# Kernel tuning notes

Hardware: AMD Instinct MI355X
Metric: run time of the kernel (lower is better)

The kernel has to match this reference:

```python
import jax, jax.numpy as jnp
import numpy as np

B, N, D_IN, D_OUT, H, W = 2, 2048, 1024, 1024, 16, 64
DH = D_OUT // H


def setup_inputs() -> dict:
    key = jax.random.key(0)
    ks = jax.random.split(key, 6)
    x = jax.random.normal(ks[0], (B, N, D_IN), dtype=jnp.float32)
    s_in = 1.0 / np.sqrt(D_IN)
    s_out = 1.0 / np.sqrt(D_OUT)
    wq = jax.random.normal(ks[1], (D_IN, D_OUT), dtype=jnp.float32) * s_in
    wk = jax.random.normal(ks[2], (D_IN, D_OUT), dtype=jnp.float32) * s_in
    wv = jax.random.normal(ks[3], (D_IN, D_OUT), dtype=jnp.float32) * s_in
    wo = jax.random.normal(ks[4], (D_OUT, D_OUT), dtype=jnp.float32) * s_out
    # sparse global tokens: every 256th token is global
    global_attention = (jnp.arange(N)[None, :] % 256 == 0) & jnp.ones((B, 1), bool)
    return {"x": x, "wq": wq, "wk": wk, "wv": wv, "wo": wo,
            "global_attention": global_attention}


def _mask(global_attention):
    # True = masked out. Causal local window + global rows/cols unmasked.
    i = jnp.arange(N)[:, None]
    j = jnp.arange(N)[None, :]
    allowed = (i - j < W) & (i >= j)          # causal sliding window
    local_mask = ~allowed                      # [N, N], True = masked
    g = global_attention                       # [B, N] bool
    # global token j clears row j and column j of the mask
    global_clear = g[:, :, None] | g[:, None, :]   # [B, N, N]
    return local_mask[None, :, :] & ~global_clear  # [B, N, N]


def reference(x, wq, wk, wv, wo, global_attention):
    b, n, _ = x.shape
    q = (x @ wq).reshape(b, n, H, DH).transpose(0, 2, 1, 3)  # [b,h,n,dh]
    k = (x @ wk).reshape(b, n, H, DH).transpose(0, 2, 1, 3)
    v = (x @ wv).reshape(b, n, H, DH).transpose(0, 2, 1, 3)
    scores = jnp.einsum('bhqd,bhkd->bhqk', q, k) / jnp.sqrt(jnp.float32(DH))
    mask = _mask(global_attention)[:, None, :, :]            # [b,1,n,n]
    scores = jnp.where(mask, -jnp.inf, scores)
    attn = jax.nn.softmax(scores, axis=-1)
    ctx = jnp.einsum('bhqk,bhkd->bqhd', attn, v).reshape(b, n, D_OUT)
    return ctx @ wo
```

## Files before the change

### kernel.cpp

```cpp
#include <hip/hip_runtime.h>


using u16 = unsigned short;
using u32 = unsigned int;

typedef __attribute__((ext_vector_type(8))) short bf16x8;
typedef __attribute__((ext_vector_type(4))) float f32x4;

__device__ __forceinline__ float b2f(u16 s) {
  union { u32 u; float f; } x; x.u = ((u32)s) << 16; return x.f;
}
__device__ __forceinline__ u16 f2b(float f) {
  union { float f; u32 u; } x; x.f = f;
  u32 r = (x.u + 0x7fffu + ((x.u >> 16) & 1u)) >> 16;
  return (u16)r;
}

__global__ __launch_bounds__(256) void k_pre(const float* __restrict__ x,
                                             u16* __restrict__ xb,
                                             const float* __restrict__ wq,
                                             const float* __restrict__ wk,
                                             const float* __restrict__ wv,
                                             const float* __restrict__ wo,
                                             u16* __restrict__ wqkvT,
                                             u16* __restrict__ woT) {
  __shared__ float tile[64][65];
  const int bid = blockIdx.x;
  if (bid < 2048) {
    int idx = (bid * 256 + threadIdx.x) * 8;
    float4 a = *(const float4*)(x + idx);
    float4 b = *(const float4*)(x + idx + 4);
    uint4 o;
    o.x = (u32)f2b(a.x) | ((u32)f2b(a.y) << 16);
    o.y = (u32)f2b(a.z) | ((u32)f2b(a.w) << 16);
    o.z = (u32)f2b(b.x) | ((u32)f2b(b.y) << 16);
    o.w = (u32)f2b(b.z) | ((u32)f2b(b.w) << 16);
    *(uint4*)(xb + idx) = o;
  } else {
    const int id = bid - 2048;
    const int z = id >> 8, xy = id & 255;
    const float* src = (z == 0) ? wq : (z == 1) ? wk : (z == 2) ? wv : wo;
    u16* dst = (z < 3) ? (wqkvT + ((size_t)z << 20)) : woT;
    const int n0 = (xy & 15) * 64, k0 = (xy >> 4) * 64;
    const int tx = threadIdx.x & 63, ty = threadIdx.x >> 6;
    #pragma unroll
    for (int r = 0; r < 64; r += 4)
      tile[r + ty][tx] = src[(size_t)(k0 + r + ty) * 1024 + n0 + tx];
    __syncthreads();
    #pragma unroll
    for (int r = 0; r < 64; r += 4)
      dst[(size_t)(n0 + r + ty) * 1024 + k0 + tx] = f2b(tile[tx][r + ty]);
  }
}

__device__ __forceinline__ void gload16(const u16* g, u16* l) {
  __builtin_amdgcn_global_load_lds((const __attribute__((address_space(1))) void*)g,
                                   (__attribute__((address_space(3))) void*)l, 16, 0, 0);
}

__global__ __launch_bounds__(512, 2) void k_qkv256(const u16* __restrict__ A,
                                                   const u16* __restrict__ Bt,
                                                   u16* __restrict__ C) {
  __shared__ __attribute__((aligned(16))) u16 lds[65536];
  const int K = 1024, N = 3072, NT = 16;
  const int t = threadIdx.x;
  const int wid = t >> 6, lane = t & 63;
  const int l4 = lane >> 4, l16 = lane & 15;
  const int qr = wid >> 2, qc = wid & 3;
  const int d = blockIdx.y * gridDim.x + blockIdx.x;
  const int qq = (gridDim.x * gridDim.y) >> 3;
  const int tau = (d & 7) * qq + (d >> 3);
  const int bn = tau % gridDim.x, bm = tau / gridDim.x;
  const u16* Ab = A + (size_t)bm * 256 * K;
  const u16* Bb = Bt + (size_t)bn * 256 * K;
  const int rowbase = wid * 8 + (lane >> 3);
  const int scc = ((lane & 7) ^ ((lane >> 3) & 7)) << 3;
  const int sdst = wid << 6;
  const int rsw = (l16 & 7);
  f32x4 acc[2][2][4][2] = {};
  bf16x8 af[4][2], bf0[2][2], bf1[2][2];

  #define STG(G, BUF, KT, H)                                                       \
    { const u16* gb = (G) ? Bb : Ab;                                               \
      u16* lb = lds + ((G) ? 32768 : 0) + (BUF) * 16384 + ((H) * 1024 + sdst) * 8; \
      _Pragma("unroll")                                                            \
      for (int i = 0; i < 2; ++i)                                                  \
        gload16(gb + (size_t)((H) * 128 + i * 64 + rowbase) * K + (KT) * 64 + scc, \
                lb + i * 4096); }

  #define LOAD_A(AS, MH)                                                           \
    { _Pragma("unroll")                                                            \
      for (int m = 0; m < 4; ++m) {                                                \
        const int ro = (MH) * 128 + qr * 64 + m * 16 + l16;                        \
        _Pragma("unroll")                                                          \
        for (int ks = 0; ks < 2; ++ks)                                             \
          af[m][ks] = *(const bf16x8*)&(AS)[ro * 64 + (((ks * 4 + l4) ^ rsw) << 3)]; \
      } }

  #define LOAD_B(BS, BF, NH)                                                       \
    { _Pragma("unroll")                                                            \
      for (int n = 0; n < 2; ++n) {                                                \
        const int ro = (NH) * 128 + qc * 32 + n * 16 + l16;                        \
        _Pragma("unroll")                                                          \
        for (int ks = 0; ks < 2; ++ks)                                             \
          BF[n][ks] = *(const bf16x8*)&(BS)[ro * 64 + (((ks * 4 + l4) ^ rsw) << 3)]; \
      } }

  #define QUAD(MH, NH, BF)                                                         \
    { __builtin_amdgcn_s_setprio(1);                                               \
      _Pragma("unroll")                                                            \
      for (int m = 0; m < 4; ++m)                                                  \
        _Pragma("unroll")                                                          \
        for (int n = 0; n < 2; ++n) {                                              \
          f32x4 c = acc[MH][NH][m][n];                                             \
          c = __builtin_amdgcn_mfma_f32_16x16x32_bf16(af[m][0], BF[n][0], c, 0, 0, 0); \
          c = __builtin_amdgcn_mfma_f32_16x16x32_bf16(af[m][1], BF[n][1], c, 0, 0, 0); \
          acc[MH][NH][m][n] = c;                                                   \
        }                                                                          \
      __builtin_amdgcn_s_setprio(0); }

  STG(0, 0, 0, 0); STG(1, 0, 0, 0); STG(0, 0, 0, 1); STG(1, 0, 0, 1);
  STG(0, 1, 1, 0); STG(1, 1, 1, 0);
  asm volatile("s_waitcnt vmcnt(4)" ::: "memory");
  __builtin_amdgcn_s_barrier();

  for (int tt = 0; tt < NT; ++tt) {
    const int beta = tt & 1;
    const u16* As = lds + beta * 16384;
    const u16* Bs = lds + 32768 + beta * 16384;
    LOAD_A(As, 0);
    LOAD_B(Bs, bf0, 0);
    if (tt + 1 < NT) STG(0, beta ^ 1, tt + 1, 1);
    __builtin_amdgcn_s_barrier();
    QUAD(0, 0, bf0);
    __builtin_amdgcn_s_barrier();
    LOAD_B(Bs, bf1, 1);
    if (tt + 1 < NT) STG(1, beta ^ 1, tt + 1, 1);
    __builtin_amdgcn_s_barrier();
    QUAD(0, 1, bf1);
    __builtin_amdgcn_s_barrier();
    LOAD_A(As, 1);
    if (tt + 2 < NT) STG(0, beta, tt + 2, 0);
    __builtin_amdgcn_s_barrier();
    QUAD(1, 0, bf0);
    __builtin_amdgcn_s_barrier();
    if (tt + 2 < NT) STG(1, beta, tt + 2, 0);
    __builtin_amdgcn_s_barrier();
    QUAD(1, 1, bf1);
    if (tt + 2 < NT)      asm volatile("s_waitcnt vmcnt(4)" ::: "memory");
    else if (tt + 1 < NT) asm volatile("s_waitcnt vmcnt(0)" ::: "memory");
    __builtin_amdgcn_s_barrier();
  }
  #undef STG
  #undef LOAD_A
  #undef LOAD_B
  #undef QUAD

  #pragma unroll
  for (int mh = 0; mh < 2; ++mh)
    #pragma unroll
    for (int m = 0; m < 4; ++m) {
      const int row0 = bm * 256 + mh * 128 + qr * 64 + m * 16 + l4 * 4;
      #pragma unroll
      for (int nh = 0; nh < 2; ++nh)
        #pragma unroll
        for (int n = 0; n < 2; ++n) {
          const int col = bn * 256 + nh * 128 + qc * 32 + n * 16 + l16;
          #pragma unroll
          for (int r = 0; r < 4; ++r)
            C[(size_t)(row0 + r) * N + col] = f2b(acc[mh][nh][m][n][r]);
        }
    }
}

template<int F32OUT, int GRED>
__global__ __launch_bounds__(256, 2) void k_gemm64(const u16* __restrict__ A,
                                                   const u16* __restrict__ Bt,
                                                   void* __restrict__ C, int N, int K,
                                                   const float* __restrict__ gpart,
                                                   u16* __restrict__ ctxw) {
  __shared__ u16 lds[3][6144];
  const int t = threadIdx.x;
  const int wid = t >> 6, lane = t & 63;
  const int l4 = lane >> 4, l16 = lane & 15;
  const int wr = wid >> 1, wc = wid & 1;
  const int d = blockIdx.y * gridDim.x + blockIdx.x;
  const int qq = (gridDim.x * gridDim.y) >> 3;
  const int tau = (d & 7) * qq + (d >> 3);
  const int bn = tau % gridDim.x, bm = tau / gridDim.x;
  const u16* Ab = A + (size_t)bm * 64 * K;
  const u16* Bb = Bt + (size_t)bn * 128 * K;
  const int srow0 = t >> 2;
  const int scol = (((t & 3) ^ ((t >> 3) & 3)) << 3);
  const int sdst = wid << 9;
  const int sl8 = ((l4 ^ ((l16 >> 1) & 3)) << 3);
  const int NT = K >> 5;
  f32x4 acc[2][4] = {};

  if (GRED && (bm & 3) == 0) {
    const int bb = bm >> 5;
    const int irow = (bm & 31) * 64;
    const int row8 = (bm & 31) >> 2;
    const int h = t >> 4;
    const int d0 = (t & 15) * 4;
    const float* g0 = gpart + ((size_t)(bb * 16 + h) * 32) * 520;
    float o0 = 0.f, o1 = 0.f, o2 = 0.f, o3 = 0.f, ls = 0.f;
    for (int q = 0; q < 32; ++q) {
      const float4 v = *(const float4*)(g0 + q * 520 + row8 * 64 + d0);
      o0 += v.x; o1 += v.y; o2 += v.z; o3 += v.w;
      ls += g0[q * 520 + 512 + row8];
    }
    const float inv = 1.f / ls;
    u16* cw = ctxw + ((size_t)(bb * 2048 + irow)) * 1024 + h * 64 + d0;
    cw[0] = f2b(o0 * inv); cw[1] = f2b(o1 * inv);
    cw[2] = f2b(o2 * inv); cw[3] = f2b(o3 * inv);
    __syncthreads();
  }

  #pragma unroll
  for (int pt = 0; pt < 2; ++pt) {
    gload16(Ab + (size_t)srow0 * K + (pt << 5) + scol, &lds[pt][sdst]);
    #pragma unroll
    for (int c = 0; c < 2; ++c)
      gload16(Bb + (size_t)(c * 64 + srow0) * K + (pt << 5) + scol,
              &lds[pt][2048 + c * 2048 + sdst]);
  }

  int cur = 0, nxt2 = 2;
  for (int tt = 0; tt < NT; ++tt) {
    if (tt + 1 < NT) asm volatile("s_waitcnt vmcnt(3)" ::: "memory");
    else             asm volatile("s_waitcnt vmcnt(0)" ::: "memory");
    __builtin_amdgcn_s_barrier();
    if (tt + 2 < NT) {
      const int k0 = (tt + 2) << 5;
      u16* dst = &lds[nxt2][0];
      gload16(Ab + (size_t)srow0 * K + k0 + scol, dst + sdst);
      #pragma unroll
      for (int c = 0; c < 2; ++c)
        gload16(Bb + (size_t)(c * 64 + srow0) * K + k0 + scol, dst + 2048 + c * 2048 + sdst);
    }
    const u16* As = lds[cur];
    const u16* Bs = lds[cur] + 2048;
    bf16x8 af[2], bf[4];
    #pragma unroll
    for (int m = 0; m < 2; ++m)
      af[m] = *(const bf16x8*)&As[(wr * 32 + m * 16 + l16) * 32 + sl8];
    #pragma unroll
    for (int n = 0; n < 4; ++n)
      bf[n] = *(const bf16x8*)&Bs[(wc * 64 + n * 16 + l16) * 32 + sl8];
    __builtin_amdgcn_s_setprio(1);
    #pragma unroll
    for (int m = 0; m < 2; ++m)
      #pragma unroll
      for (int n = 0; n < 4; ++n)
        acc[m][n] = __builtin_amdgcn_mfma_f32_16x16x32_bf16(af[m], bf[n], acc[m][n], 0, 0, 0);
    __builtin_amdgcn_s_setprio(0);
    cur = (cur == 2) ? 0 : cur + 1;
    nxt2 = (nxt2 == 2) ? 0 : nxt2 + 1;
  }

  #pragma unroll
  for (int m = 0; m < 2; ++m) {
    const int row0 = bm * 64 + wr * 32 + m * 16 + l4 * 4;
    #pragma unroll
    for (int n = 0; n < 4; ++n) {
      const int col = bn * 128 + wc * 64 + n * 16 + l16;
      #pragma unroll
      for (int r = 0; r < 4; ++r) {
        if (F32OUT) ((float*)C)[(size_t)(row0 + r) * N + col] = acc[m][n][r];
        else        ((u16*)C)[(size_t)(row0 + r) * N + col] = f2b(acc[m][n][r]);
      }
    }
  }
}

__global__ __launch_bounds__(256) void k_attn_tile(const u16* __restrict__ qkv,
                                                   u16* __restrict__ ctx,
                                                   float* __restrict__ gpart) {
  __shared__ u16 buf[26880];
  __shared__ u16 Qgs[16 * 72];
  __shared__ u16 Pgs[16 * 72];
  __shared__ float lred[4][16];
  u16* Qs = buf;
  u16* Ks = buf + 4608;
  u16* Vt = buf + 16128;
  u16* Ps = buf;

  const int t = threadIdx.x, wid = t >> 6, lane = t & 63;
  const int l4 = lane >> 4, l16 = lane & 15;
  const int qt = blockIdx.x, h = blockIdx.y, b = blockIdx.z;
  const int q0 = qt * 64;
  const int kbase = q0 - 64;
  const size_t base = (size_t)b * 2048 * 3072;
  const u16* Qg = qkv + base + h * 64;
  const u16* Kg = qkv + base + 1024 + h * 64;
  const u16* Vg = qkv + base + 2048 + h * 64;

  for (int s = t; s < 512; s += 256) {
    int r = s >> 3, c = (s & 7) * 8;
    *(uint4*)&Qs[r * 72 + c] = *(const uint4*)&Qg[(size_t)(q0 + r) * 3072 + c];
  }
  if (t < 128) {
    int r = t >> 3, c = (t & 7) * 8;
    if (r < 8) {
      *(uint4*)&Qgs[r * 72 + c] = *(const uint4*)&Qg[(size_t)(r * 256) * 3072 + c];
    } else {
      uint4 z = {0, 0, 0, 0};
      *(uint4*)&Qgs[r * 72 + c] = z;
    }
  }
  for (int s = t; s < 1088; s += 256) {
    int r = s >> 3, c = (s & 7) * 8;
    int j = (r < 128) ? max(kbase + r, 0) : (r - 128) * 256;
    *(uint4*)&Ks[r * 72 + c] = *(const uint4*)&Kg[(size_t)j * 3072 + c];
  }
  for (int s = t; s < 1088; s += 256) {
    int r = s >> 3, c = (s & 7) * 8;
    int j = (r < 128) ? max(kbase + r, 0) : (r - 128) * 256;
    uint4 v = *(const uint4*)&Vg[(size_t)j * 3072 + c];
    const u16* pv = (const u16*)&v;
    const int ch = r >> 3;
    #pragma unroll
    for (int e8 = 0; e8 < 8; ++e8) {
      const int d = c + e8;
      const int kd = ((d >> 3) ^ d) & 7;
      const int chs = (ch < 16) ? (ch ^ kd) : ch;
      Vt[d * 168 + chs * 8 + (r & 7)] = pv[e8];
    }
  }
  for (int z = t; z < 64 * 24; z += 256) {
    int d = z / 24, j = 136 + z % 24;
    Vt[d * 168 + j] = 0;
  }
  __syncthreads();

  f32x4 sa[10] = {};
  #pragma unroll
  for (int ks = 0; ks < 2; ++ks) {
    bf16x8 qa = *(const bf16x8*)&Qs[(wid * 16 + l16) * 72 + ks * 32 + l4 * 8];
    #pragma unroll
    for (int n = 0; n < 10; ++n) {
      bf16x8 kb = *(const bf16x8*)&Ks[(n * 16 + l16) * 72 + ks * 32 + l4 * 8];
      sa[n] = __builtin_amdgcn_mfma_f32_16x16x32_bf16(qa, kb, sa[n], 0, 0, 0);
    }
  }

  f32x4 sg = {};
  #pragma unroll
  for (int ks = 0; ks < 2; ++ks) {
    bf16x8 qa = *(const bf16x8*)&Qgs[l16 * 72 + ks * 32 + l4 * 8];
    bf16x8 kb = *(const bf16x8*)&Ks[(64 + wid * 16 + l16) * 72 + ks * 32 + l4 * 8];
    sg = __builtin_amdgcn_mfma_f32_16x16x32_bf16(qa, kb, sg, 0, 0, 0);
  }
  #pragma unroll
  for (int r = 0; r < 4; ++r) {
    float p = __expf(sg[r] * 0.125f);
    sg[r] = p;
    #pragma unroll
    for (int o = 1; o < 16; o <<= 1) p += __shfl_xor(p, o);
    if (l16 == 0) lred[wid][l4 * 4 + r] = p;
  }
  #pragma unroll
  for (int r = 0; r < 4; ++r)
    Pgs[(l4 * 4 + r) * 72 + wid * 16 + l16] = f2b(sg[r]);

  const int qi0 = wid * 16 + l4 * 4;
  #pragma unroll
  for (int n = 0; n < 10; ++n) {
    const int jc = n * 16 + l16;
    #pragma unroll
    for (int r = 0; r < 4; ++r) {
      const int qi = qi0 + r;
      bool allowed;
      if (n < 8) {
        const int kr = kbase + jc;
        allowed = (jc > qi) && (jc <= qi + 64) && (kr >= 0) && ((kr & 255) != 0);
      } else {
        allowed = (jc < 136);
      }
      sa[n][r] = allowed ? sa[n][r] * 0.125f : -1e30f;
    }
  }

  float m[4], l[4];
  #pragma unroll
  for (int r = 0; r < 4; ++r) {
    float mx = sa[0][r];
    #pragma unroll
    for (int n = 1; n < 10; ++n) mx = fmaxf(mx, sa[n][r]);
    #pragma unroll
    for (int o = 1; o < 16; o <<= 1) mx = fmaxf(mx, __shfl_xor(mx, o));
    m[r] = mx;
    l[r] = 0.f;
  }
  #pragma unroll
  for (int n = 0; n < 10; ++n)
    #pragma unroll
    for (int r = 0; r < 4; ++r) {
      float p = __expf(sa[n][r] - m[r]);
      sa[n][r] = p;
      l[r] += p;
    }
  #pragma unroll
  for (int r = 0; r < 4; ++r)
    #pragma unroll
    for (int o = 1; o < 16; o <<= 1) l[r] += __shfl_xor(l[r], o);

  __syncthreads();

  u16* Pw = Ps + wid * (16 * 168);
  #pragma unroll
  for (int n = 0; n < 10; ++n)
    #pragma unroll
    for (int r = 0; r < 4; ++r)
      Pw[(l4 * 4 + r) * 168 + n * 16 + l16] = f2b(sa[n][r]);
  __syncthreads();

  f32x4 o[4] = {};
  #pragma unroll
  for (int ks = 0; ks < 5; ++ks) {
    bf16x8 pa = *(const bf16x8*)&Pw[l16 * 168 + ks * 32 + l4 * 8];
    #pragma unroll
    for (int dt = 0; dt < 4; ++dt) {
      const int dvo = dt * 16 + l16;
      const int kdo = ((dvo >> 3) ^ dvo) & 7;
      const int ch = ks * 4 + l4;
      const int chs = (ch < 16) ? (ch ^ kdo) : ch;
      bf16x8 vb = *(const bf16x8*)&Vt[dvo * 168 + chs * 8];
      o[dt] = __builtin_amdgcn_mfma_f32_16x16x32_bf16(pa, vb, o[dt], 0, 0, 0);
    }
  }

  f32x4 og = {};
  {
    const int dV = wid * 16 + l16;
    const int kdg = ((dV >> 3) ^ dV) & 7;
    #pragma unroll
    for (int ks = 0; ks < 2; ++ks) {
      bf16x8 pa = *(const bf16x8*)&Pgs[l16 * 72 + ks * 32 + l4 * 8];
      const int chs = (8 + ks * 4 + l4) ^ kdg;
      bf16x8 vb = *(const bf16x8*)&Vt[dV * 168 + chs * 8];
      og = __builtin_amdgcn_mfma_f32_16x16x32_bf16(pa, vb, og, 0, 0, 0);
    }
  }
  float* gp = gpart + ((size_t)(b * 16 + h) * 32 + qt) * 520;
  #pragma unroll
  for (int r = 0; r < 4; ++r) {
    int row = l4 * 4 + r;
    if (row < 8) gp[row * 64 + wid * 16 + l16] = og[r];
  }
  if (t < 8) gp[512 + t] = lred[0][t] + lred[1][t] + lred[2][t] + lred[3][t];

  #pragma unroll
  for (int r = 0; r < 4; ++r) {
    const int q = q0 + qi0 + r;
    if ((q & 255) == 0) continue;
    const float inv = 1.0f / l[r];
    #pragma unroll
    for (int dt = 0; dt < 4; ++dt)
      ctx[(size_t)(b * 2048 + q) * 1024 + h * 64 + dt * 16 + l16] = f2b(o[dt][r] * inv);
  }
}

extern "C" void kernel_launch(void* const* d_in, const int* in_sizes, int n_in,
                              void* d_out, int out_size, void* d_ws, size_t ws_size,
                              hipStream_t stream) {
  (void)in_sizes; (void)n_in; (void)out_size; (void)ws_size;
  const float* x  = (const float*)d_in[0];
  const float* wq = (const float*)d_in[1];
  const float* wk = (const float*)d_in[2];
  const float* wv = (const float*)d_in[3];
  const float* wo = (const float*)d_in[4];
  char* ws = (char*)d_ws;
  u16* xb    = (u16*)(ws);
  u16* qkv   = (u16*)(ws + (8u  << 20));
  u16* ctx   = (u16*)(ws + (32u << 20));
  u16* wqkvT = (u16*)(ws + (40u << 20));
  u16* woT   = (u16*)(ws + (46u << 20));
  float* gpart = (float*)(ws);

  k_pre<<<3072, 256, 0, stream>>>(x, xb, wq, wk, wv, wo, wqkvT, woT);
  k_qkv256<<<dim3(12, 16), 512, 0, stream>>>(xb, wqkvT, qkv);
  k_attn_tile<<<dim3(32, 16, 2), 256, 0, stream>>>(qkv, ctx, gpart);
  k_gemm64<1, 1><<<dim3(8, 64), 256, 0, stream>>>(ctx, woT, d_out, 1024, 1024, gpart, ctx);
}
```

Baseline: 86.63 us.

## Retile QKV GEMM to 256x192 blocks for a 256-block grid

The QKV projection GEMM now uses 256x192 output tiles instead of 256x256, which gives a 16x16 grid of 256 blocks in place of 192. The wave layout changes to 4x2 and each wave covers 64 rows by 96 columns in three column sub-steps. The B staging, LDS buffer sizes, wait counts and epilogue are reworked to match. The aim is to fill the 256 CUs of the MI355X in a single wave, at the cost of reusing each A tile across fewer columns and running a different pipeline schedule.

```diff
diff --git a/kernel.cpp b/kernel.cpp
--- a/kernel.cpp
+++ b/kernel.cpp
@@ -61,115 +61,119 @@
 __global__ __launch_bounds__(512, 2) void k_qkv256(const u16* __restrict__ A,
                                                    const u16* __restrict__ Bt,
                                                    u16* __restrict__ C) {
-  __shared__ __attribute__((aligned(16))) u16 lds[65536];
+  __shared__ __attribute__((aligned(16))) u16 lds[57344];
   const int K = 1024, N = 3072, NT = 16;
   const int t = threadIdx.x;
   const int wid = t >> 6, lane = t & 63;
   const int l4 = lane >> 4, l16 = lane & 15;
-  const int qr = wid >> 2, qc = wid & 3;
+  const int qr = wid >> 1, qc = wid & 1;
   const int d = blockIdx.y * gridDim.x + blockIdx.x;
   const int qq = (gridDim.x * gridDim.y) >> 3;
   const int tau = (d & 7) * qq + (d >> 3);
   const int bn = tau % gridDim.x, bm = tau / gridDim.x;
   const u16* Ab = A + (size_t)bm * 256 * K;
-  const u16* Bb = Bt + (size_t)bn * 256 * K;
+  const u16* Bb = Bt + (size_t)bn * 192 * K;
   const int rowbase = wid * 8 + (lane >> 3);
+  const int qcg = rowbase >> 5, rrb = rowbase & 31;
   const int scc = ((lane & 7) ^ ((lane >> 3) & 7)) << 3;
-  const int sdst = wid << 6;
   const int rsw = (l16 & 7);
-  f32x4 acc[2][2][4][2] = {};
-  bf16x8 af[4][2], bf0[2][2], bf1[2][2];
-
-  #define STG(G, BUF, KT, H)                                                       \
-    { const u16* gb = (G) ? Bb : Ab;                                               \
-      u16* lb = lds + ((G) ? 32768 : 0) + (BUF) * 16384 + ((H) * 1024 + sdst) * 8; \
+  f32x4 acc[3][4][2] = {};
+  bf16x8 af[4][2], bf[2][2];
+
+  #define STG_A(BUF, KT, H)                                                        \
+    { u16* lb = lds + (BUF) * 16384 + (H) * 8192 + (wid << 9);                     \
       _Pragma("unroll")                                                            \
       for (int i = 0; i < 2; ++i)                                                  \
-        gload16(gb + (size_t)((H) * 128 + i * 64 + rowbase) * K + (KT) * 64 + scc, \
+        gload16(Ab + (size_t)((H) * 128 + i * 64 + rowbase) * K + (KT) * 64 + scc, \
                 lb + i * 4096); }
 
-  #define LOAD_A(AS, MH)                                                           \
+  #define STG_B1(BUF, KT, I)                                                       \
+    { u16* lb = lds + 32768 + (BUF) * 12288 + (I) * 4096 + (wid << 9);             \
+      gload16(Bb + (size_t)(qcg * 96 + (I) * 32 + rrb) * K + (KT) * 64 + scc, lb); }
+
+  #define LOAD_A(AS)                                                               \
     { _Pragma("unroll")                                                            \
       for (int m = 0; m < 4; ++m) {                                                \
-        const int ro = (MH) * 128 + qr * 64 + m * 16 + l16;                        \
+        const int ro = qr * 64 + m * 16 + l16;                                     \
         _Pragma("unroll")                                                          \
         for (int ks = 0; ks < 2; ++ks)                                             \
           af[m][ks] = *(const bf16x8*)&(AS)[ro * 64 + (((ks * 4 + l4) ^ rsw) << 3)]; \
       } }
 
-  #define LOAD_B(BS, BF, NH)                                                       \
+  #define LOAD_B(BS, NH)                                                           \
     { _Pragma("unroll")                                                            \
       for (int n = 0; n < 2; ++n) {                                                \
-        const int ro = (NH) * 128 + qc * 32 + n * 16 + l16;                        \
+        const int po = (NH) * 64 + qc * 32 + n * 16 + l16;                         \
         _Pragma("unroll")                                                          \
         for (int ks = 0; ks < 2; ++ks)                                             \
-          BF[n][ks] = *(const bf16x8*)&(BS)[ro * 64 + (((ks * 4 + l4) ^ rsw) << 3)]; \
+          bf[n][ks] = *(const bf16x8*)&(BS)[po * 64 + (((ks * 4 + l4) ^ rsw) << 3)]; \
       } }
 
-  #define QUAD(MH, NH, BF)                                                         \
+  #define QUAD(NH)                                                                 \
     { __builtin_amdgcn_s_setprio(1);                                               \
       _Pragma("unroll")                                                            \
       for (int m = 0; m < 4; ++m)                                                  \
         _Pragma("unroll")                                                          \
         for (int n = 0; n < 2; ++n) {                                              \
-          f32x4 c = acc[MH][NH][m][n];                                             \
-          c = __builtin_amdgcn_mfma_f32_16x16x32_bf16(af[m][0], BF[n][0], c, 0, 0, 0); \
-          c = __builtin_amdgcn_mfma_f32_16x16x32_bf16(af[m][1], BF[n][1], c, 0, 0, 0); \
-          acc[MH][NH][m][n] = c;                                                   \
+          f32x4 c = acc[NH][m][n];                                                 \
+          c = __builtin_amdgcn_mfma_f32_16x16x32_bf16(af[m][0], bf[n][0], c, 0, 0, 0); \
+          c = __builtin_amdgcn_mfma_f32_16x16x32_bf16(af[m][1], bf[n][1], c, 0, 0, 0); \
+          acc[NH][m][n] = c;                                                       \
         }                                                                          \
       __builtin_amdgcn_s_setprio(0); }
 
-  STG(0, 0, 0, 0); STG(1, 0, 0, 0); STG(0, 0, 0, 1); STG(1, 0, 0, 1);
-  STG(0, 1, 1, 0); STG(1, 1, 1, 0);
-  asm volatile("s_waitcnt vmcnt(4)" ::: "memory");
+  STG_A(0, 0, 0); STG_A(0, 0, 1);
+  STG_B1(0, 0, 0); STG_B1(0, 0, 1); STG_B1(0, 0, 2);
+  STG_A(1, 1, 0); STG_A(1, 1, 1);
+  STG_B1(1, 1, 0);
+  asm volatile("s_waitcnt vmcnt(5)" ::: "memory");
   __builtin_amdgcn_s_barrier();
 
   for (int tt = 0; tt < NT; ++tt) {
     const int beta = tt & 1;
     const u16* As = lds + beta * 16384;
-    const u16* Bs = lds + 32768 + beta * 16384;
-    LOAD_A(As, 0);
-    LOAD_B(Bs, bf0, 0);
-    if (tt + 1 < NT) STG(0, beta ^ 1, tt + 1, 1);
-    __builtin_amdgcn_s_barrier();
-    QUAD(0, 0, bf0);
-    __builtin_amdgcn_s_barrier();
-    LOAD_B(Bs, bf1, 1);
-    if (tt + 1 < NT) STG(1, beta ^ 1, tt + 1, 1);
-    __builtin_amdgcn_s_barrier();
-    QUAD(0, 1, bf1);
-    __builtin_amdgcn_s_barrier();
-    LOAD_A(As, 1);
-    if (tt + 2 < NT) STG(0, beta, tt + 2, 0);
-    __builtin_amdgcn_s_barrier();
-    QUAD(1, 0, bf0);
-    __builtin_amdgcn_s_barrier();
-    if (tt + 2 < NT) STG(1, beta, tt + 2, 0);
-    __builtin_amdgcn_s_barrier();
-    QUAD(1, 1, bf1);
-    if (tt + 2 < NT)      asm volatile("s_waitcnt vmcnt(4)" ::: "memory");
+    const u16* Bs = lds + 32768 + beta * 12288;
+    LOAD_A(As);
+    LOAD_B(Bs, 0);
+    if (tt + 1 < NT) STG_B1(beta ^ 1, tt + 1, 1);
+    __builtin_amdgcn_s_barrier();
+    QUAD(0);
+    __builtin_amdgcn_s_barrier();
+    LOAD_B(Bs, 1);
+    if (tt + 1 < NT) STG_B1(beta ^ 1, tt + 1, 2);
+    __builtin_amdgcn_s_barrier();
+    QUAD(1);
+    __builtin_amdgcn_s_barrier();
+    LOAD_B(Bs, 2);
+    if (tt + 2 < NT) {
+      STG_A(beta, tt + 2, 0);
+      STG_A(beta, tt + 2, 1);
+      STG_B1(beta, tt + 2, 0);
+    }
+    __builtin_amdgcn_s_barrier();
+    QUAD(2);
+    if (tt + 2 < NT)      asm volatile("s_waitcnt vmcnt(5)" ::: "memory");
     else if (tt + 1 < NT) asm volatile("s_waitcnt vmcnt(0)" ::: "memory");
     __builtin_amdgcn_s_barrier();
   }
-  #undef STG
+  #undef STG_A
+  #undef STG_B1
   #undef LOAD_A
   #undef LOAD_B
   #undef QUAD
 
   #pragma unroll
-  for (int mh = 0; mh < 2; ++mh)
+  for (int nh = 0; nh < 3; ++nh)
     #pragma unroll
     for (int m = 0; m < 4; ++m) {
-      const int row0 = bm * 256 + mh * 128 + qr * 64 + m * 16 + l4 * 4;
+      const int row0 = bm * 256 + qr * 64 + m * 16 + l4 * 4;
       #pragma unroll
-      for (int nh = 0; nh < 2; ++nh)
+      for (int n = 0; n < 2; ++n) {
+        const int col = bn * 192 + qc * 96 + nh * 32 + n * 16 + l16;
         #pragma unroll
-        for (int n = 0; n < 2; ++n) {
-          const int col = bn * 256 + nh * 128 + qc * 32 + n * 16 + l16;
-          #pragma unroll
-          for (int r = 0; r < 4; ++r)
-            C[(size_t)(row0 + r) * N + col] = f2b(acc[mh][nh][m][n][r]);
-        }
+        for (int r = 0; r < 4; ++r)
+          C[(size_t)(row0 + r) * N + col] = f2b(acc[nh][m][n][r]);
+      }
     }
 }
 
@@ -480,7 +484,7 @@
   float* gpart = (float*)(ws);
 
   k_pre<<<3072, 256, 0, stream>>>(x, xb, wq, wk, wv, wo, wqkvT, woT);
-  k_qkv256<<<dim3(12, 16), 512, 0, stream>>>(xb, wqkvT, qkv);
+  k_qkv256<<<dim3(16, 16), 512, 0, stream>>>(xb, wqkvT, qkv);
   k_attn_tile<<<dim3(32, 16, 2), 256, 0, stream>>>(qkv, ctx, gpart);
   k_gemm64<1, 1><<<dim3(8, 64), 256, 0, stream>>>(ctx, woT, d_out, 1024, 1024, gpart, ctx);
 }
```

Result: faster. 82.94 us (-4.3%).
